# Kernel tuning notes

Measured on AMD Instinct MI355X. Metric: run time of the kernel, lower is better.

Reference implementation:

```python
import jax, jax.numpy as jnp
from jax import lax
import numpy as np

B, N, C, NPOINT, K = 8, 4096, 64, 1024, 32
EPS = 1e-5
SLOPE = 0.1  # leakyrelu negative_slope


def setup_inputs() -> dict:
    key = jax.random.key(0)
    ks = jax.random.split(key, 8)
    d = {
        "xyz": jax.random.normal(ks[0], (B, N, 3), jnp.float32),
        "features": jax.random.normal(ks[1], (B, N, C), jnp.float32),
    }
    for i, n in enumerate(["w_t", "w1_0", "w2_0", "w1_1", "w2_1"]):
        d[n] = jax.random.normal(ks[2 + i], (C, C), jnp.float32) * 0.05
    for n in ["b_t", "b1_0", "b2_0", "b1_1", "b2_1"]:
        d[n] = jnp.zeros((C,), jnp.float32)
    for n in ["g_t", "g1_0", "g2_0", "g1_1", "g2_1"]:
        d[n] = jnp.ones((C,), jnp.float32)
    for n in ["beta_t", "beta1_0", "beta2_0", "beta1_1", "beta2_1"]:
        d[n] = jnp.zeros((C,), jnp.float32)
    return d


def leaky(x):
    return jnp.where(x >= 0, x, SLOPE * x)


def conv1(x, w, b):  # x: [M, Cin, K], w: [Cout, Cin] (1x1 conv)
    return jnp.einsum('mck,oc->mok', x, w) + b[None, :, None]


def bn(x, g, be):  # training-mode BatchNorm1d over (batch, spatial)
    mean = x.mean(axis=(0, 2), keepdims=True)
    var = x.var(axis=(0, 2), keepdims=True)
    return g[None, :, None] * (x - mean) / jnp.sqrt(var + EPS) + be[None, :, None]


def fps(xyz, npoint):
    """Farthest point sampling, deterministic start at index 0. -> [B, npoint] int32"""
    b, n, _ = xyz.shape
    def step(carry, _):
        dist, far = carry
        centroid = jnp.take_along_axis(xyz, far[:, None, None], axis=1)  # [B,1,3]
        d = jnp.sum((xyz - centroid) ** 2, -1)  # [B,N]
        dist = jnp.minimum(dist, d)
        return (dist, jnp.argmax(dist, -1)), far
    init = (jnp.full((b, n), 1e10, xyz.dtype), jnp.zeros((b,), jnp.int32))
    _, idxs = lax.scan(step, init, None, length=npoint)  # [npoint, B]
    return idxs.T


def sqdist(src, dst):  # [B,S,3],[B,N,3] -> [B,S,N]
    d = -2.0 * jnp.einsum('bsc,bnc->bsn', src, dst)
    d += jnp.sum(src ** 2, -1)[:, :, None]
    d += jnp.sum(dst ** 2, -1)[:, None, :]
    return d


def resblock(x, w1, b1, g1, be1, w2, b2, g2, be2):
    h = leaky(bn(conv1(x, w1, b1), g1, be1))
    h = bn(conv1(h, w2, b2), g2, be2)
    return leaky(h + x)


def reference(xyz, features, w_t, b_t, g_t, beta_t,
              w1_0, b1_0, g1_0, beta1_0, w2_0, b2_0, g2_0, beta2_0,
              w1_1, b1_1, g1_1, beta1_1, w2_1, b2_1, g2_1, beta2_1):
    fps_idx = fps(xyz, NPOINT)                                   # [B,S]
    new_xyz = jnp.take_along_axis(xyz, fps_idx[:, :, None], axis=1)  # [B,S,3]
    d = sqdist(new_xyz, xyz)                                     # [B,S,N]
    _, idx = lax.top_k(-d, K)                                    # k smallest -> [B,S,K]
    grouped = jax.vmap(lambda f, i: f[i])(features, idx)         # [B,S,K,C]
    x = grouped.transpose(0, 1, 3, 2).reshape(B * NPOINT, C, K)  # [B*S, C, K]
    x = leaky(bn(conv1(x, w_t, b_t), g_t, beta_t))
    x = resblock(x, w1_0, b1_0, g1_0, beta1_0, w2_0, b2_0, g2_0, beta2_0)
    x = resblock(x, w1_1, b1_1, g1_1, beta1_1, w2_1, b2_1, g2_1, beta2_1)
    nf = x.reshape(B, NPOINT, C, K).transpose(0, 2, 1, 3)        # [B,C,S,K]
    sub_features = nf.max(axis=-1)                               # [B,C,S]
    return (new_xyz.transpose(0, 2, 1), sub_features)
```

## Files before the change

kernel.cpp:

```cpp
#include <hip/hip_runtime.h>
#include <stdint.h>

#define NB 8
#define NN 4096
#define NC 64
#define NS 1024
#define NK 32
#define NQ (NB*NS)
#define NP (NQ*NK)
#define EPSBN 1e-5f

typedef unsigned long long u64;
typedef unsigned short u16;
typedef float v2f __attribute__((ext_vector_type(2)));
typedef short bf8_t __attribute__((ext_vector_type(8)));
typedef float f4_t __attribute__((ext_vector_type(4)));

__device__ __forceinline__ float lrelu(float x){ return x >= 0.0f ? x : 0.1f*x; }

__device__ __forceinline__ unsigned int fkey(float d){
    unsigned int fb = __float_as_uint(d);
    return (fb & 0x80000000u) ? ~fb : (fb | 0x80000000u);
}
__device__ __forceinline__ unsigned f2bf(float f){
    unsigned u = __float_as_uint(f);
    return (u + 0x7fffu + ((u >> 16) & 1u)) >> 16;
}
__device__ __forceinline__ float bflo(unsigned u){ return __uint_as_float(u << 16); }
__device__ __forceinline__ float bfhi(unsigned u){ return __uint_as_float(u & 0xffff0000u); }

__device__ __forceinline__ int wave_incl_add(int x){
    int v = x;
    {int o=__builtin_amdgcn_update_dpp(0,v,0x111,0xf,0xf,true); v+=o;}
    {int o=__builtin_amdgcn_update_dpp(0,v,0x112,0xf,0xf,true); v+=o;}
    {int o=__builtin_amdgcn_update_dpp(0,v,0x114,0xf,0xf,true); v+=o;}
    {int o=__builtin_amdgcn_update_dpp(0,v,0x118,0xf,0xf,true); v+=o;}
    {int o=__builtin_amdgcn_update_dpp(0,v,0x142,0xa,0xf,true); v+=o;}
    {int o=__builtin_amdgcn_update_dpp(0,v,0x143,0xc,0xf,true); v+=o;}
    return v;
}
__device__ __forceinline__ float row_sum16(float x){
    int v = __float_as_int(x);
    {int o=__builtin_amdgcn_update_dpp(0,v,0x111,0xf,0xf,true); v=__float_as_int(__int_as_float(v)+__int_as_float(o));}
    {int o=__builtin_amdgcn_update_dpp(0,v,0x112,0xf,0xf,true); v=__float_as_int(__int_as_float(v)+__int_as_float(o));}
    {int o=__builtin_amdgcn_update_dpp(0,v,0x114,0xf,0xf,true); v=__float_as_int(__int_as_float(v)+__int_as_float(o));}
    {int o=__builtin_amdgcn_update_dpp(0,v,0x118,0xf,0xf,true); v=__float_as_int(__int_as_float(v)+__int_as_float(o));}
    return __int_as_float(v);
}
__device__ __forceinline__ double wave_max_d(double x){
    int lo = __double2loint(x), hi = __double2hiint(x);
    #define FPS_STG(ctl) { \
        int nl=__builtin_amdgcn_update_dpp(lo,lo,ctl,0xf,0xf,false); \
        int nh=__builtin_amdgcn_update_dpp(hi,hi,ctl,0xf,0xf,false); \
        double mx=fmax(__hiloint2double(hi,lo), __hiloint2double(nh,nl)); \
        lo=__double2loint(mx); hi=__double2hiint(mx); }
    FPS_STG(0x111) FPS_STG(0x112) FPS_STG(0x114) FPS_STG(0x118) FPS_STG(0x142) FPS_STG(0x143)
    #undef FPS_STG
    int flo = __builtin_amdgcn_readlane(lo, 63);
    int fhi = __builtin_amdgcn_readlane(hi, 63);
    return __hiloint2double(fhi, flo);
}

__global__ __launch_bounds__(256,1) void fps_kernel(const float* __restrict__ xyz,
    float* __restrict__ out0, float* __restrict__ nxyz,
    const float* __restrict__ features, u16* __restrict__ fbf,
    const float* __restrict__ w0, const float* __restrict__ w1,
    const float* __restrict__ w2, const float* __restrict__ w3,
    const float* __restrict__ w4, u16* __restrict__ bwt)
{
    if (blockIdx.x >= NB + 512){
        const int wb = blockIdx.x - (NB + 512);
        const float* s;
        switch (wb){
            case 0: s = w0; break; case 1: s = w1; break; case 2: s = w2; break;
            case 3: s = w3; break; default: s = w4; break;
        }
        u16* d = bwt + (size_t)wb*4096;
        for (int i = threadIdx.x; i < 4096; i += 256){
            const int f = i >> 9, lane = (i >> 3) & 63, j = i & 7;
            const int mt = f >> 1, h = f & 1;
            const int o = mt*16 + (lane & 15);
            const int c = h*32 + (lane >> 4)*8 + j;
            d[i] = (u16)f2bf(s[o*64 + c]);
        }
        return;
    }
    if (blockIdx.x >= NB){
        const int cb = blockIdx.x - NB;
        const float4* src = (const float4*)features;
        uint2* dst = (uint2*)fbf;
        for (int i = cb*256 + threadIdx.x; i < NB*NN*NC/4; i += 512*256){
            float4 v = src[i];
            uint2 pk;
            pk.x = f2bf(v.x) | (f2bf(v.y) << 16);
            pk.y = f2bf(v.z) | (f2bf(v.w) << 16);
            dst[i] = pk;
        }
        return;
    }
    __shared__ float sX[NN], sY[NN], sZ[NN];
    __shared__ double slots[2][4];
    __shared__ int sFar[NS];
    const int b = blockIdx.x, t = threadIdx.x;
    const int lane = t & 63, wv = t >> 6;
    const float* base = xyz + (size_t)b*NN*3;
    for (int i = t; i < NN; i += 256){
        const float* pp = base + 3*i;
        sX[i] = pp[0]; sY[i] = pp[1]; sZ[i] = pp[2];
    }
    __syncthreads();
    v2f PX[8], PY[8], PZ[8], D[8];
    int LO[16];
    const int pb = t*16;
    #pragma unroll
    for (int j = 0; j < 8; ++j){
        PX[j] = (v2f){ sX[pb+2*j], sX[pb+2*j+1] };
        PY[j] = (v2f){ sY[pb+2*j], sY[pb+2*j+1] };
        PZ[j] = (v2f){ sZ[pb+2*j], sZ[pb+2*j+1] };
        D[j]  = (v2f){ 1e10f, 1e10f };
    }
    #pragma unroll
    for (int j = 0; j < 16; ++j) LO[j] = (int)(~(unsigned)(pb + j));
    int far = 0;
    float cx = sX[0], cy = sY[0], cz = sZ[0];
    for (int s = 0; s < NS; ++s){
        if (t == 255) sFar[s] = far;
        double best;
        {
            #pragma clang fp contract(off)
            v2f cx2 = (v2f){cx, cx}, cy2 = (v2f){cy, cy}, cz2 = (v2f){cz, cz};
            best = -1.0;
            #pragma unroll
            for (int j = 0; j < 8; ++j){
                v2f dx = PX[j] - cx2;
                v2f dy = PY[j] - cy2;
                v2f dz = PZ[j] - cz2;
                v2f dd = (dx*dx + dy*dy) + dz*dz;
                v2f nd = __builtin_elementwise_min(D[j], dd);
                D[j] = nd;
                best = fmax(best, __hiloint2double(__float_as_int(nd.x), LO[2*j]));
                best = fmax(best, __hiloint2double(__float_as_int(nd.y), LO[2*j+1]));
            }
        }
        double wb = wave_max_d(best);
        const int par = s & 1;
        if (lane == 0) slots[par][wv] = wb;
        __syncthreads();
        double s0 = slots[par][0], s1 = slots[par][1];
        double s2 = slots[par][2], s3 = slots[par][3];
        double mm = fmax(fmax(s0, s1), fmax(s2, s3));
        far = (int)(~(unsigned)__double2loint(mm));
        cx = sX[far]; cy = sY[far]; cz = sZ[far];
    }
    __syncthreads();
    for (int s = t; s < NS; s += 256){
        const int f = sFar[s];
        const float x = sX[f], y = sY[f], z = sZ[f];
        float* npq = nxyz + ((size_t)b*NS + s)*3;
        npq[0]=x; npq[1]=y; npq[2]=z;
        out0[(b*3+0)*NS+s]=x; out0[(b*3+1)*NS+s]=y; out0[(b*3+2)*NS+s]=z;
    }
}

__global__ __launch_bounds__(256,2) void knn_kernel(const float* __restrict__ xyz,
                                                    const float* __restrict__ nxyz,
                                                    int* __restrict__ kidx)
{
    const int t = threadIdx.x, lane = t & 63, w = t >> 6;
    const int q = blockIdx.x*4 + w;
    const int b = q >> 10;
    const float* base = xyz + (size_t)b*NN*3;
    const float* qp = nxyz + (size_t)q*3;
    const float qx = qp[0], qy = qp[1], qz = qp[2];
    const float qsq = __fadd_rn(__fadd_rn(__fmul_rn(qx,qx),__fmul_rn(qy,qy)),__fmul_rn(qz,qz));

    unsigned int key[64];
    #pragma unroll
    for (int i = 0; i < 64; ++i){
        const int idx = (i<<6) + lane;
        const float* pp = base + 3*idx;
        float x = pp[0], y = pp[1], z = pp[2];
        float dot = __fadd_rn(__fadd_rn(__fmul_rn(qx,x),__fmul_rn(qy,y)),__fmul_rn(qz,z));
        float psq = __fadd_rn(__fadd_rn(__fmul_rn(x,x),__fmul_rn(y,y)),__fmul_rn(z,z));
        float d = __fadd_rn(__fadd_rn(__fmul_rn(-2.0f,dot),qsq),psq);
        key[i] = fkey(d);
    }
    unsigned int pref = 0; int need = 32;
    for (int bit = 31; bit >= 0; --bit){
        const unsigned int bound = 1u << bit;
        int c = 0;
        #pragma unroll
        for (int i = 0; i < 64; ++i) c += ((key[i] ^ pref) < bound) ? 1 : 0;
        int tot = __builtin_amdgcn_readlane(wave_incl_add(c), 63);
        if (tot < need){ need -= tot; pref |= bound; }
    }
    const unsigned int T = pref;
    int cl = 0;
    #pragma unroll
    for (int i = 0; i < 64; ++i) cl += (key[i] < T) ? 1 : 0;
    int incl_cl = wave_incl_add(cl);
    int clx = incl_cl - cl;
    int tiebase = __builtin_amdgcn_readlane(incl_cl, 63);
    int* oq = kidx + (size_t)q*NK;
    int pos = clx;
    #pragma unroll
    for (int i = 0; i < 64; ++i){
        if (key[i] < T){ oq[pos] = (i<<6) + lane; ++pos; }
    }
    int tcount = 0;
    for (int i = 0; i < 64 && tcount < need; ++i){
        u64 m = __ballot(key[i] == T);
        int myrank = (int)__popcll(m & ((1ull << lane) - 1ull));
        if ((key[i] == T) && (tcount + myrank < need))
            oq[tiebase + tcount + myrank] = (i<<6) + lane;
        tcount += (int)__popcll(m);
    }
}

__global__ __launch_bounds__(1024) void finalize_kernel(const float* __restrict__ pin,
    const float* __restrict__ g, const float* __restrict__ beta, float* __restrict__ aff)
{
    __shared__ float l1[1024];
    const int t = threadIdx.x;
    const int stat = t & 127, seg = t >> 7;
    float S = 0.0f;
    #pragma unroll 8
    for (int r = seg*128; r < seg*128 + 128; ++r) S += pin[r*128 + stat];
    l1[t] = S;
    __syncthreads();
    if (t < 128){
        float s = l1[t] + l1[128+t] + l1[256+t] + l1[384+t]
                + l1[512+t] + l1[640+t] + l1[768+t] + l1[896+t];
        l1[t] = s;
    }
    __syncthreads();
    if (t < 64){
        float mean = l1[t] * (1.0f/(float)NP);
        float var  = fmaxf(l1[64+t] * (1.0f/(float)NP) - mean*mean, 0.0f);
        float sc = g[t] * rsqrtf(var + EPSBN);
        aff[t]    = sc;
        aff[64+t] = beta[t] - mean*sc;
    }
}

template<int ACT>
__global__ __launch_bounds__(256, (ACT==2)?2:3) void conv_mfma_kernel(
    const u16* __restrict__ in, const u16* __restrict__ in2,
    u16* __restrict__ out, u16* __restrict__ x2out,
    const u16* __restrict__ wfrag, const float* __restrict__ bias,
    const float* __restrict__ aff, const float* __restrict__ aff2,
    float* __restrict__ pout)
{
    __shared__ float sStat[4*128];
    const int t = threadIdx.x, lane = t & 63, wv = t >> 6;
    const int n = lane & 15, q = lane >> 4;
    const int bb = blockIdx.x;

    float scr[16], shr[16];
    float scr2[16], shr2[16];
    if (ACT){
        #pragma unroll
        for (int h = 0; h < 2; ++h){
            float4 a0 = *(const float4*)(aff + h*32 + q*8);
            float4 a1 = *(const float4*)(aff + h*32 + q*8 + 4);
            float4 b0 = *(const float4*)(aff + 64 + h*32 + q*8);
            float4 b1 = *(const float4*)(aff + 64 + h*32 + q*8 + 4);
            scr[h*8+0]=a0.x; scr[h*8+1]=a0.y; scr[h*8+2]=a0.z; scr[h*8+3]=a0.w;
            scr[h*8+4]=a1.x; scr[h*8+5]=a1.y; scr[h*8+6]=a1.z; scr[h*8+7]=a1.w;
            shr[h*8+0]=b0.x; shr[h*8+1]=b0.y; shr[h*8+2]=b0.z; shr[h*8+3]=b0.w;
            shr[h*8+4]=b1.x; shr[h*8+5]=b1.y; shr[h*8+6]=b1.z; shr[h*8+7]=b1.w;
        }
        if (ACT == 2){
            #pragma unroll
            for (int h = 0; h < 2; ++h){
                float4 a0 = *(const float4*)(aff2 + h*32 + q*8);
                float4 a1 = *(const float4*)(aff2 + h*32 + q*8 + 4);
                float4 b0 = *(const float4*)(aff2 + 64 + h*32 + q*8);
                float4 b1 = *(const float4*)(aff2 + 64 + h*32 + q*8 + 4);
                scr2[h*8+0]=a0.x; scr2[h*8+1]=a0.y; scr2[h*8+2]=a0.z; scr2[h*8+3]=a0.w;
                scr2[h*8+4]=a1.x; scr2[h*8+5]=a1.y; scr2[h*8+6]=a1.z; scr2[h*8+7]=a1.w;
                shr2[h*8+0]=b0.x; shr2[h*8+1]=b0.y; shr2[h*8+2]=b0.z; shr2[h*8+3]=b0.w;
                shr2[h*8+4]=b1.x; shr2[h*8+5]=b1.y; shr2[h*8+6]=b1.z; shr2[h*8+7]=b1.w;
            }
        }
    }
    bf8_t wf[8];
    #pragma unroll
    for (int f = 0; f < 8; ++f)
        wf[f] = *(const bf8_t*)(wfrag + (f*64 + lane)*8);
    f4_t bv[4];
    #pragma unroll
    for (int mt = 0; mt < 4; ++mt)
        bv[mt] = *(const f4_t*)(bias + mt*16 + q*4);

    float st1[16], st2[16];
    #pragma unroll
    for (int e = 0; e < 16; ++e){ st1[e] = 0.0f; st2[e] = 0.0f; }

    #pragma unroll
    for (int i = 0; i < 4; ++i){
        const int p0 = bb*256 + wv*64 + i*16;
        const u16* row = in + (size_t)(p0 + n)*64;
        bf8_t bf0, bf1;
        union { unsigned u[4]; bf8_t v; } B0, B1;
        if (ACT == 1){
            uint4 r0 = *(const uint4*)(row + q*8);
            uint4 r1 = *(const uint4*)(row + 32 + q*8);
            const unsigned ra[4] = {r0.x, r0.y, r0.z, r0.w};
            const unsigned rb[4] = {r1.x, r1.y, r1.z, r1.w};
            #pragma unroll
            for (int d = 0; d < 4; ++d){
                float x0 = bflo(ra[d]), x1 = bfhi(ra[d]);
                float y0 = fmaf(scr[2*d],   x0, shr[2*d]);   y0 = lrelu(y0);
                float y1 = fmaf(scr[2*d+1], x1, shr[2*d+1]); y1 = lrelu(y1);
                B0.u[d] = f2bf(y0) | (f2bf(y1) << 16);
                float z0 = bflo(rb[d]), z1 = bfhi(rb[d]);
                float w0 = fmaf(scr[8+2*d],   z0, shr[8+2*d]);   w0 = lrelu(w0);
                float w1 = fmaf(scr[8+2*d+1], z1, shr[8+2*d+1]); w1 = lrelu(w1);
                B1.u[d] = f2bf(w0) | (f2bf(w1) << 16);
            }
            bf0 = B0.v; bf1 = B1.v;
        } else if (ACT == 2){
            const u16* yrow = in2 + (size_t)(p0 + n)*64;
            uint4 r0 = *(const uint4*)(row + q*8);
            uint4 r1 = *(const uint4*)(row + 32 + q*8);
            uint4 s0 = *(const uint4*)(yrow + q*8);
            uint4 s1 = *(const uint4*)(yrow + 32 + q*8);
            const unsigned ra[4] = {r0.x, r0.y, r0.z, r0.w};
            const unsigned rb[4] = {r1.x, r1.y, r1.z, r1.w};
            const unsigned ya[4] = {s0.x, s0.y, s0.z, s0.w};
            const unsigned yb[4] = {s1.x, s1.y, s1.z, s1.w};
            #pragma unroll
            for (int d = 0; d < 4; ++d){
                float t0 = lrelu(fmaf(scr2[2*d],   bflo(ya[d]), shr2[2*d]));
                float t1 = lrelu(fmaf(scr2[2*d+1], bfhi(ya[d]), shr2[2*d+1]));
                float x0 = lrelu(fmaf(scr[2*d],    bflo(ra[d]), shr[2*d])   + t0);
                float x1 = lrelu(fmaf(scr[2*d+1],  bfhi(ra[d]), shr[2*d+1]) + t1);
                B0.u[d] = f2bf(x0) | (f2bf(x1) << 16);
                float u0 = lrelu(fmaf(scr2[8+2*d],   bflo(yb[d]), shr2[8+2*d]));
                float u1 = lrelu(fmaf(scr2[8+2*d+1], bfhi(yb[d]), shr2[8+2*d+1]));
                float v0 = lrelu(fmaf(scr[8+2*d],    bflo(rb[d]), shr[8+2*d])   + u0);
                float v1 = lrelu(fmaf(scr[8+2*d+1],  bfhi(rb[d]), shr[8+2*d+1]) + u1);
                B1.u[d] = f2bf(v0) | (f2bf(v1) << 16);
            }
            u16* xrow = x2out + (size_t)(p0 + n)*64;
            *(uint4*)(xrow + q*8)      = (uint4){B0.u[0],B0.u[1],B0.u[2],B0.u[3]};
            *(uint4*)(xrow + 32 + q*8) = (uint4){B1.u[0],B1.u[1],B1.u[2],B1.u[3]};
            bf0 = B0.v; bf1 = B1.v;
        } else {
            bf0 = *(const bf8_t*)(row + q*8);
            bf1 = *(const bf8_t*)(row + 32 + q*8);
        }
        f4_t acc[4];
        #pragma unroll
        for (int mt = 0; mt < 4; ++mt){
            acc[mt] = (f4_t){0.f,0.f,0.f,0.f};
            acc[mt] = __builtin_amdgcn_mfma_f32_16x16x32_bf16(wf[mt*2+0], bf0, acc[mt], 0,0,0);
            acc[mt] = __builtin_amdgcn_mfma_f32_16x16x32_bf16(wf[mt*2+1], bf1, acc[mt], 0,0,0);
        }
        u16* orow = out + (size_t)(p0 + n)*64;
        #pragma unroll
        for (int mt = 0; mt < 4; ++mt){
            float v0 = acc[mt].x + bv[mt].x;
            float v1 = acc[mt].y + bv[mt].y;
            float v2 = acc[mt].z + bv[mt].z;
            float v3 = acc[mt].w + bv[mt].w;
            st1[mt*4+0] += v0; st2[mt*4+0] += v0*v0;
            st1[mt*4+1] += v1; st2[mt*4+1] += v1*v1;
            st1[mt*4+2] += v2; st2[mt*4+2] += v2*v2;
            st1[mt*4+3] += v3; st2[mt*4+3] += v3*v3;
            uint2 pk;
            pk.x = f2bf(v0) | (f2bf(v1) << 16);
            pk.y = f2bf(v2) | (f2bf(v3) << 16);
            *(uint2*)(orow + mt*16 + q*4) = pk;
        }
    }
    #pragma unroll
    for (int e = 0; e < 16; ++e){
        float r1 = row_sum16(st1[e]);
        float r2 = row_sum16(st2[e]);
        if (n == 15){
            const int ch = (e >> 2)*16 + q*4 + (e & 3);
            sStat[wv*128 + ch]      = r1;
            sStat[wv*128 + 64 + ch] = r2;
        }
    }
    __syncthreads();
    if (t < 128){
        float s = sStat[t] + sStat[128+t] + sStat[256+t] + sStat[384+t];
        pout[(size_t)bb*128 + t] = s;
    }
}

__global__ __launch_bounds__(256,3) void gconv_mfma_kernel(const u16* __restrict__ fbf,
    const int* __restrict__ kidx, u16* __restrict__ out,
    const u16* __restrict__ wfrag, const float* __restrict__ bias,
    float* __restrict__ pout)
{
    __shared__ float sStat[4*128];
    const int t = threadIdx.x, lane = t & 63, wv = t >> 6;
    const int n = lane & 15, q = lane >> 4;
    const int bb = blockIdx.x;

    bf8_t wf[8];
    #pragma unroll
    for (int f = 0; f < 8; ++f)
        wf[f] = *(const bf8_t*)(wfrag + (f*64 + lane)*8);
    f4_t bv[4];
    #pragma unroll
    for (int mt = 0; mt < 4; ++mt)
        bv[mt] = *(const f4_t*)(bias + mt*16 + q*4);

    float st1[16], st2[16];
    #pragma unroll
    for (int e = 0; e < 16; ++e){ st1[e] = 0.0f; st2[e] = 0.0f; }

    #pragma unroll
    for (int i = 0; i < 4; ++i){
        const int p0 = bb*256 + wv*64 + i*16;
        const int p = p0 + n;
        const int b = p >> 15;
        const int idx = kidx[p];
        const u16* frow = fbf + ((size_t)b*NN + idx)*NC;
        bf8_t bf0 = *(const bf8_t*)(frow + q*8);
        bf8_t bf1 = *(const bf8_t*)(frow + 32 + q*8);
        f4_t acc[4];
        #pragma unroll
        for (int mt = 0; mt < 4; ++mt){
            acc[mt] = (f4_t){0.f,0.f,0.f,0.f};
            acc[mt] = __builtin_amdgcn_mfma_f32_16x16x32_bf16(wf[mt*2+0], bf0, acc[mt], 0,0,0);
            acc[mt] = __builtin_amdgcn_mfma_f32_16x16x32_bf16(wf[mt*2+1], bf1, acc[mt], 0,0,0);
        }
        u16* orow = out + (size_t)p*64;
        #pragma unroll
        for (int mt = 0; mt < 4; ++mt){
            float v0 = acc[mt].x + bv[mt].x;
            float v1 = acc[mt].y + bv[mt].y;
            float v2 = acc[mt].z + bv[mt].z;
            float v3 = acc[mt].w + bv[mt].w;
            st1[mt*4+0] += v0; st2[mt*4+0] += v0*v0;
            st1[mt*4+1] += v1; st2[mt*4+1] += v1*v1;
            st1[mt*4+2] += v2; st2[mt*4+2] += v2*v2;
            st1[mt*4+3] += v3; st2[mt*4+3] += v3*v3;
            uint2 pk;
            pk.x = f2bf(v0) | (f2bf(v1) << 16);
            pk.y = f2bf(v2) | (f2bf(v3) << 16);
            *(uint2*)(orow + mt*16 + q*4) = pk;
        }
    }
    #pragma unroll
    for (int e = 0; e < 16; ++e){
        float r1 = row_sum16(st1[e]);
        float r2 = row_sum16(st2[e]);
        if (n == 15){
            const int ch = (e >> 2)*16 + q*4 + (e & 3);
            sStat[wv*128 + ch]      = r1;
            sStat[wv*128 + 64 + ch] = r2;
        }
    }
    __syncthreads();
    if (t < 128){
        float s = sStat[t] + sStat[128+t] + sStat[256+t] + sStat[384+t];
        pout[(size_t)bb*128 + t] = s;
    }
}

__global__ __launch_bounds__(256,2) void final_kernel(const u16* __restrict__ v2,
    const u16* __restrict__ x2, const float* __restrict__ aff,
    float* __restrict__ out1)
{
    const int t = threadIdx.x;
    const int dc = t & 31, sg = t >> 5;
    const int c0 = dc*2, c1 = c0 + 1;
    const float a0 = aff[c0], s0 = aff[64+c0];
    const float a1 = aff[c1], s1 = aff[64+c1];
    const int s = blockIdx.x*8 + sg;
    const unsigned* vp = (const unsigned*)v2;
    const unsigned* xp = (const unsigned*)x2;
    float m0 = -3.0e38f, m1 = -3.0e38f;
    #pragma unroll 8
    for (int kk = 0; kk < 32; ++kk){
        const size_t e = ((size_t)s*32 + kk)*32 + dc;
        unsigned uv = vp[e], ux = xp[e];
        m0 = fmaxf(m0, lrelu(fmaf(a0, bflo(uv), s0) + bflo(ux)));
        m1 = fmaxf(m1, lrelu(fmaf(a1, bfhi(uv), s1) + bfhi(ux)));
    }
    const int b = s >> 10, sl = s & 1023;
    out1[((size_t)b*NC + c0)*NS + sl] = m0;
    out1[((size_t)b*NC + c1)*NS + sl] = m1;
}

extern "C" void kernel_launch(void* const* d_in, const int* in_sizes, int n_in,
                              void* d_out, int out_size, void* d_ws, size_t ws_size,
                              hipStream_t stream)
{
    const float* xyz      = (const float*)d_in[0];
    const float* features = (const float*)d_in[1];
    const float* w_t    = (const float*)d_in[2];
    const float* w1_0   = (const float*)d_in[3];
    const float* w2_0   = (const float*)d_in[4];
    const float* w1_1   = (const float*)d_in[5];
    const float* w2_1   = (const float*)d_in[6];
    const float* b_t    = (const float*)d_in[7];
    const float* b1_0   = (const float*)d_in[8];
    const float* b2_0   = (const float*)d_in[9];
    const float* b1_1   = (const float*)d_in[10];
    const float* b2_1   = (const float*)d_in[11];
    const float* g_t    = (const float*)d_in[12];
    const float* g1_0   = (const float*)d_in[13];
    const float* g2_0   = (const float*)d_in[14];
    const float* g1_1   = (const float*)d_in[15];
    const float* g2_1   = (const float*)d_in[16];
    const float* beta_t  = (const float*)d_in[17];
    const float* beta1_0 = (const float*)d_in[18];
    const float* beta2_0 = (const float*)d_in[19];
    const float* beta1_1 = (const float*)d_in[20];
    const float* beta2_1 = (const float*)d_in[21];

    float* out = (float*)d_out;

    float* nxyz = (float*)d_ws;
    int*   kidx = (int*)(nxyz + 24576);
    float* pT   = (float*)(kidx + NP);
    float* p10  = pT  + 131072;
    float* p20  = p10 + 131072;
    float* p11  = p20 + 131072;
    float* p21  = p11 + 131072;
    float* affT  = p21 + 131072;
    float* aff10 = affT + 128;
    float* aff20 = aff10 + 128;
    float* aff11 = aff20 + 128;
    float* aff21 = aff11 + 128;
    u16*  bwt  = (u16*)(aff21 + 128);
    u16*  buf0 = bwt + 5*4096;
    u16*  buf1 = buf0 + (size_t)NP*NC;
    u16*  buf2 = buf1 + (size_t)NP*NC;
    u16*  fbf  = buf2;

    fps_kernel<<<NB + 512 + 5, 256, 0, stream>>>(xyz, out, nxyz, features, fbf,
                                                 w_t, w1_0, w2_0, w1_1, w2_1, bwt);
    knn_kernel<<<NQ/4, 256, 0, stream>>>(xyz, nxyz, kidx);

    gconv_mfma_kernel<<<1024, 256, 0, stream>>>(fbf, kidx, buf1,
                                                bwt + 0*4096, b_t, pT);
    finalize_kernel<<<1, 1024, 0, stream>>>(pT, g_t, beta_t, affT);
    conv_mfma_kernel<1><<<1024, 256, 0, stream>>>(buf1, nullptr, buf0, nullptr,
                                                  bwt + 1*4096, b1_0, affT, nullptr, p10);
    finalize_kernel<<<1, 1024, 0, stream>>>(p10, g1_0, beta1_0, aff10);
    conv_mfma_kernel<1><<<1024, 256, 0, stream>>>(buf0, nullptr, buf2, nullptr,
                                                  bwt + 2*4096, b2_0, aff10, nullptr, p20);
    finalize_kernel<<<1, 1024, 0, stream>>>(p20, g2_0, beta2_0, aff20);
    conv_mfma_kernel<2><<<1024, 256, 0, stream>>>(buf2, buf1, buf1, buf0,
                                                  bwt + 3*4096, b1_1, aff20, affT, p11);
    finalize_kernel<<<1, 1024, 0, stream>>>(p11, g1_1, beta1_1, aff11);
    conv_mfma_kernel<1><<<1024, 256, 0, stream>>>(buf1, nullptr, buf2, nullptr,
                                                  bwt + 4*4096, b2_1, aff11, nullptr, p21);
    finalize_kernel<<<1, 1024, 0, stream>>>(p21, g2_1, beta2_1, aff21);
    final_kernel<<<1024, 256, 0, stream>>>(buf2, buf0, aff21,
                                           out + (size_t)NB*3*NS);
}
```

Before: 905.1 us.

## Process two batches per FPS block to overlap serial reduction latency

Each FPS block now handles two batch elements at once, interleaving their distance updates and wave reductions and sharing one barrier per step. The serial per-iteration latency of reduction and synchronization is meant to be amortized over two independent chains. This halves the number of FPS blocks and doubles LDS and register use per block, which risks spills or longer per-step compute.

Result: slower. 1.334 ms (+47.4%).

```diff
diff --git a/kernel.cpp b/kernel.cpp
--- a/kernel.cpp
+++ b/kernel.cpp
@@ -68,8 +68,8 @@
     const float* __restrict__ w2, const float* __restrict__ w3,
     const float* __restrict__ w4, u16* __restrict__ bwt)
 {
-    if (blockIdx.x >= NB + 512){
-        const int wb = blockIdx.x - (NB + 512);
+    if (blockIdx.x >= 4 + 512){
+        const int wb = blockIdx.x - (4 + 512);
         const float* s;
         switch (wb){
             case 0: s = w0; break; case 1: s = w1; break; case 2: s = w2; break;
@@ -85,8 +85,8 @@
         }
         return;
     }
-    if (blockIdx.x >= NB){
-        const int cb = blockIdx.x - NB;
+    if (blockIdx.x >= 4){
+        const int cb = blockIdx.x - 4;
         const float4* src = (const float4*)features;
         uint2* dst = (uint2*)fbf;
         for (int i = cb*256 + threadIdx.x; i < NB*NN*NC/4; i += 512*256){
@@ -98,67 +98,115 @@
         }
         return;
     }
-    __shared__ float sX[NN], sY[NN], sZ[NN];
-    __shared__ double slots[2][4];
-    __shared__ int sFar[NS];
-    const int b = blockIdx.x, t = threadIdx.x;
+    __shared__ float sXA[NN], sYA[NN], sZA[NN];
+    __shared__ float sXB[NN], sYB[NN], sZB[NN];
+    __shared__ double slotsA[2][4], slotsB[2][4];
+    __shared__ int sFarA[NS], sFarB[NS];
+    const int t = threadIdx.x;
     const int lane = t & 63, wv = t >> 6;
-    const float* base = xyz + (size_t)b*NN*3;
+    const int bA = blockIdx.x*2, bB = bA + 1;
+    const float* baseA = xyz + (size_t)bA*NN*3;
+    const float* baseB = xyz + (size_t)bB*NN*3;
     for (int i = t; i < NN; i += 256){
-        const float* pp = base + 3*i;
-        sX[i] = pp[0]; sY[i] = pp[1]; sZ[i] = pp[2];
+        const float* pa = baseA + 3*i;
+        sXA[i] = pa[0]; sYA[i] = pa[1]; sZA[i] = pa[2];
+        const float* pb_ = baseB + 3*i;
+        sXB[i] = pb_[0]; sYB[i] = pb_[1]; sZB[i] = pb_[2];
     }
     __syncthreads();
-    v2f PX[8], PY[8], PZ[8], D[8];
+    v2f PXA[8], PYA[8], PZA[8], DA[8];
+    v2f PXB[8], PYB[8], PZB[8], DB[8];
     int LO[16];
     const int pb = t*16;
     #pragma unroll
     for (int j = 0; j < 8; ++j){
-        PX[j] = (v2f){ sX[pb+2*j], sX[pb+2*j+1] };
-        PY[j] = (v2f){ sY[pb+2*j], sY[pb+2*j+1] };
-        PZ[j] = (v2f){ sZ[pb+2*j], sZ[pb+2*j+1] };
-        D[j]  = (v2f){ 1e10f, 1e10f };
+        PXA[j] = (v2f){ sXA[pb+2*j], sXA[pb+2*j+1] };
+        PYA[j] = (v2f){ sYA[pb+2*j], sYA[pb+2*j+1] };
+        PZA[j] = (v2f){ sZA[pb+2*j], sZA[pb+2*j+1] };
+        DA[j]  = (v2f){ 1e10f, 1e10f };
+        PXB[j] = (v2f){ sXB[pb+2*j], sXB[pb+2*j+1] };
+        PYB[j] = (v2f){ sYB[pb+2*j], sYB[pb+2*j+1] };
+        PZB[j] = (v2f){ sZB[pb+2*j], sZB[pb+2*j+1] };
+        DB[j]  = (v2f){ 1e10f, 1e10f };
     }
     #pragma unroll
     for (int j = 0; j < 16; ++j) LO[j] = (int)(~(unsigned)(pb + j));
-    int far = 0;
-    float cx = sX[0], cy = sY[0], cz = sZ[0];
+    int farA = 0, farB = 0;
+    float cxA = sXA[0], cyA = sYA[0], czA = sZA[0];
+    float cxB = sXB[0], cyB = sYB[0], czB = sZB[0];
     for (int s = 0; s < NS; ++s){
-        if (t == 255) sFar[s] = far;
-        double best;
+        if (t == 255){ sFarA[s] = farA; sFarB[s] = farB; }
+        const int par = s & 1;
         {
-            #pragma clang fp contract(off)
-            v2f cx2 = (v2f){cx, cx}, cy2 = (v2f){cy, cy}, cz2 = (v2f){cz, cz};
-            best = -1.0;
-            #pragma unroll
-            for (int j = 0; j < 8; ++j){
-                v2f dx = PX[j] - cx2;
-                v2f dy = PY[j] - cy2;
-                v2f dz = PZ[j] - cz2;
-                v2f dd = (dx*dx + dy*dy) + dz*dz;
-                v2f nd = __builtin_elementwise_min(D[j], dd);
-                D[j] = nd;
-                best = fmax(best, __hiloint2double(__float_as_int(nd.x), LO[2*j]));
-                best = fmax(best, __hiloint2double(__float_as_int(nd.y), LO[2*j+1]));
+            double best;
+            {
+                #pragma clang fp contract(off)
+                v2f cx2 = (v2f){cxA, cxA}, cy2 = (v2f){cyA, cyA}, cz2 = (v2f){czA, czA};
+                best = -1.0;
+                #pragma unroll
+                for (int j = 0; j < 8; ++j){
+                    v2f dx = PXA[j] - cx2;
+                    v2f dy = PYA[j] - cy2;
+                    v2f dz = PZA[j] - cz2;
+                    v2f dd = (dx*dx + dy*dy) + dz*dz;
+                    v2f nd = __builtin_elementwise_min(DA[j], dd);
+                    DA[j] = nd;
+                    best = fmax(best, __hiloint2double(__float_as_int(nd.x), LO[2*j]));
+                    best = fmax(best, __hiloint2double(__float_as_int(nd.y), LO[2*j+1]));
+                }
             }
-        }
-        double wb = wave_max_d(best);
-        const int par = s & 1;
-        if (lane == 0) slots[par][wv] = wb;
+            double wb = wave_max_d(best);
+            if (lane == 0) slotsA[par][wv] = wb;
+        }
+        {
+            double best;
+            {
+                #pragma clang fp contract(off)
+                v2f cx2 = (v2f){cxB, cxB}, cy2 = (v2f){cyB, cyB}, cz2 = (v2f){czB, czB};
+                best = -1.0;
+                #pragma unroll
+                for (int j = 0; j < 8; ++j){
+                    v2f dx = PXB[j] - cx2;
+                    v2f dy = PYB[j] - cy2;
+                    v2f dz = PZB[j] - cz2;
+                    v2f dd = (dx*dx + dy*dy) + dz*dz;
+                    v2f nd = __builtin_elementwise_min(DB[j], dd);
+                    DB[j] = nd;
+                    best = fmax(best, __hiloint2double(__float_as_int(nd.x), LO[2*j]));
+                    best = fmax(best, __hiloint2double(__float_as_int(nd.y), LO[2*j+1]));
+                }
+            }
+            double wb = wave_max_d(best);
+            if (lane == 0) slotsB[par][wv] = wb;
+        }
         __syncthreads();
-        double s0 = slots[par][0], s1 = slots[par][1];
-        double s2 = slots[par][2], s3 = slots[par][3];
-        double mm = fmax(fmax(s0, s1), fmax(s2, s3));
-        far = (int)(~(unsigned)__double2loint(mm));
-        cx = sX[far]; cy = sY[far]; cz = sZ[far];
+        {
+            double s0 = slotsA[par][0], s1 = slotsA[par][1];
+            double s2 = slotsA[par][2], s3 = slotsA[par][3];
+            double mm = fmax(fmax(s0, s1), fmax(s2, s3));
+            farA = (int)(~(unsigned)__double2loint(mm));
+            cxA = sXA[farA]; cyA = sYA[farA]; czA = sZA[farA];
+        }
+        {
+            double s0 = slotsB[par][0], s1 = slotsB[par][1];
+            double s2 = slotsB[par][2], s3 = slotsB[par][3];
+            double mm = fmax(fmax(s0, s1), fmax(s2, s3));
+            farB = (int)(~(unsigned)__double2loint(mm));
+            cxB = sXB[farB]; cyB = sYB[farB]; czB = sZB[farB];
+        }
     }
     __syncthreads();
     for (int s = t; s < NS; s += 256){
-        const int f = sFar[s];
-        const float x = sX[f], y = sY[f], z = sZ[f];
-        float* npq = nxyz + ((size_t)b*NS + s)*3;
-        npq[0]=x; npq[1]=y; npq[2]=z;
-        out0[(b*3+0)*NS+s]=x; out0[(b*3+1)*NS+s]=y; out0[(b*3+2)*NS+s]=z;
+        const int fA = sFarA[s];
+        const float xA = sXA[fA], yA = sYA[fA], zA = sZA[fA];
+        float* npqA = nxyz + ((size_t)bA*NS + s)*3;
+        npqA[0]=xA; npqA[1]=yA; npqA[2]=zA;
+        out0[(bA*3+0)*NS+s]=xA; out0[(bA*3+1)*NS+s]=yA; out0[(bA*3+2)*NS+s]=zA;
+        const int fB = sFarB[s];
+        const float xB = sXB[fB], yB = sYB[fB], zB = sZB[fB];
+        float* npqB = nxyz + ((size_t)bB*NS + s)*3;
+        npqB[0]=xB; npqB[1]=yB; npqB[2]=zB;
+        out0[(bB*3+0)*NS+s]=xB; out0[(bB*3+1)*NS+s]=yB; out0[(bB*3+2)*NS+s]=zB;
     }
 }
 
@@ -537,8 +585,8 @@
     u16*  buf2 = buf1 + (size_t)NP*NC;
     u16*  fbf  = buf2;
 
-    fps_kernel<<<NB + 512 + 5, 256, 0, stream>>>(xyz, out, nxyz, features, fbf,
-                                                 w_t, w1_0, w2_0, w1_1, w2_1, bwt);
+    fps_kernel<<<4 + 512 + 5, 256, 0, stream>>>(xyz, out, nxyz, features, fbf,
+                                                w_t, w1_0, w2_0, w1_1, w2_1, bwt);
     knn_kernel<<<NQ/4, 256, 0, stream>>>(xyz, nxyz, kidx);
 
     gconv_mfma_kernel<<<1024, 256, 0, stream>>>(fbf, kidx, buf1,
```
